# Performance work log

Hardware: AMD Instinct MI355X
Metric: run time of the kernel (lower is better)

## Reference

```python
import math
import jax, jax.numpy as jnp
import numpy as np

COLORS = 10
MAX_SHIFT = 5
B, H, W = 32, 128, 128

_shifts = [(dy, dx) for dy in range(-MAX_SHIFT, MAX_SHIFT + 1)
           for dx in range(-MAX_SHIFT, MAX_SHIFT + 1)
           if not (dy == 0 and dx == 0)]  # include_identity=False
DYS = jnp.asarray(np.array([s[0] for s in _shifts], dtype=np.int32))
DXS = jnp.asarray(np.array([s[1] for s in _shifts], dtype=np.int32))


def _shift_all(grid):
    """Apply every (dy,dx) shift to an int grid [B,H,W] with zero padding.

    out[s, b, y, x] = grid[b, y-dy_s, x-dx_s] if in-bounds else 0,
    exactly matching apply_shift_batch (uncovered regions are color 0).
    Returns [S, B, H, W].
    """
    b, h, w = grid.shape
    padded = jnp.pad(grid, ((0, 0), (MAX_SHIFT, MAX_SHIFT), (MAX_SHIFT, MAX_SHIFT)))
    def one(dy, dx):
        return jax.lax.dynamic_slice(padded, (0, MAX_SHIFT - dy, MAX_SHIFT - dx), (b, h, w))
    return jax.vmap(one)(DYS, DXS)


def setup_inputs() -> dict:
    key = jax.random.key(0)
    k1, k2, k3 = jax.random.split(key, 3)
    return {
        "demo_in": jax.random.randint(k1, (B, H, W), 0, COLORS, dtype=jnp.int32),
        "demo_out": jax.random.randint(k2, (B, H, W), 0, COLORS, dtype=jnp.int32),
        "query_in": jax.random.randint(k3, (B, H, W), 0, COLORS, dtype=jnp.int32),
        "color_log_weight": jnp.zeros((COLORS,), dtype=jnp.float32),
        "logit_scale": jnp.asarray(4.0, dtype=jnp.float32),
    }


def reference(demo_in, demo_out, query_in, color_log_weight, logit_scale):
    b, h, w = query_in.shape
    S = DYS.shape[0]

    # Per-shift correlation score. one_hot(shifted)*one_hot(demo_out)*w summed
    # over (C,H,W) == sum over pixels of w[demo_out] * (shifted == demo_out).
    shifted_demo = _shift_all(demo_in)                       # [S,B,H,W] int
    w_out = jnp.exp(color_log_weight)[demo_out]              # [B,H,W]
    eq = (shifted_demo == demo_out[None]).astype(jnp.float32)
    match = jnp.sum(eq * w_out[None], axis=(2, 3))           # [S,B]
    scale = jnp.minimum(jnp.exp(logit_scale), 100.0)
    scores = match.T / math.sqrt(h * w) * scale              # [B,S]
    attention = jax.nn.softmax(scores, axis=1)               # [B,S]

    # Weighted accumulation of one-hot shifted queries, done as a scatter-add
    # into the color channel (avoids materializing [S,B,C,H,W]).
    shifted_query = _shift_all(query_in)                     # [S,B,H,W] int
    b_idx = jnp.arange(b)[None, :, None, None]
    y_idx = jnp.arange(h)[None, None, :, None]
    x_idx = jnp.arange(w)[None, None, None, :]
    attn_b = jnp.broadcast_to(attention.T[:, :, None, None], (S, b, h, w))
    accum = jnp.zeros((b, COLORS, h, w), dtype=jnp.float32)
    accum = accum.at[b_idx, shifted_query, y_idx, x_idx].add(attn_b)
    return jnp.log(jnp.maximum(accum, 1e-6))
```

## Files before the change

### kernel.cpp

```cpp
#include <hip/hip_runtime.h>
#include <hip/hip_bf16.h>
#include <math.h>

#define COLORS 10
#define NB 32
#define H 128
#define W 128
#define NS 120
#define HW (H*W)
#define STRIPS 8
#define SH 16
#define DROWS 26
#define DINW 12

typedef unsigned char u8;
typedef unsigned int u32;
typedef unsigned long long u64;
typedef float f32x4 __attribute__((ext_vector_type(4)));
typedef short bf16x8 __attribute__((ext_vector_type(8)));

__global__ __launch_bounds__(512) void match_strip(
    const int* __restrict__ demo_in, const int* __restrict__ demo_out,
    const float* __restrict__ clw, float* __restrict__ mpart)
{
    __shared__ __align__(16) u32 din_p[COLORS][DROWS][DINW];
    __shared__ __align__(16) u32 dout_p[COLORS][SH][4];
    __shared__ float wexp[COLORS];

    int t = threadIdx.x;
    int strip = blockIdx.x;
    int b = blockIdx.y;
    int wave = t >> 6, lane = t & 63;

    if (t < COLORS) wexp[t] = __expf(clw[t]);

    const int* di = demo_in  + b * HW;
    const int* dd = demo_out + b * HW;
    int y0 = strip * SH;

    for (int r = wave; r < DROWS; r += 8) {
        int gy = y0 - 5 + r;
        bool ok = (gy >= 0 && gy < H);
        int v0 = 0, v1 = 0;
        if (ok) { v0 = di[gy * W + lane]; v1 = di[gy * W + 64 + lane]; }
        #pragma unroll
        for (int c = 0; c < COLORS; c++) {
            u64 h0 = __ballot(v0 == c);
            u64 h1 = __ballot(v1 == c);
            u64 P0, P1, P2;
            if (!ok) {
                P0 = (c == 0) ? ~0ull : 0ull;
                P1 = P0;
                P2 = (c == 0) ? 0x3FFull : 0ull;
            } else {
                u64 lm = (c == 0) ? 0x1Full  : 0ull;
                u64 rm = (c == 0) ? 0x3E0ull : 0ull;
                P0 = (h0 << 5) | lm;
                P1 = (h0 >> 59) | (h1 << 5);
                P2 = (h1 >> 59) | rm;
            }
            if (lane == 0) {
                *reinterpret_cast<uint4*>(&din_p[c][r][0]) =
                    make_uint4((u32)P0, (u32)(P0 >> 32), (u32)P1, (u32)(P1 >> 32));
                *reinterpret_cast<uint4*>(&din_p[c][r][4]) =
                    make_uint4((u32)P2, 0u, 0u, 0u);
            }
        }
    }
    for (int r = wave; r < SH; r += 8) {
        int gy = y0 + r;
        int v0 = dd[gy * W + lane], v1 = dd[gy * W + 64 + lane];
        #pragma unroll
        for (int c = 0; c < COLORS; c++) {
            u64 h0 = __ballot(v0 == c);
            u64 h1 = __ballot(v1 == c);
            if (lane == 0)
                *reinterpret_cast<uint4*>(&dout_p[c][r][0]) =
                    make_uint4((u32)h0, (u32)(h0 >> 32), (u32)h1, (u32)(h1 >> 32));
        }
    }
    __syncthreads();

    int s = t >> 2, q = t & 3;
    float acc = 0.f;
    if (t < 4 * NS) {
        int lin = s + (s >= 60);
        int dy = lin / 11 - 5, dx = lin % 11 - 5;
        int k = 5 - dx;
        for (int c = 0; c < COLORS; c++) {
            int cnt = 0;
            #pragma unroll
            for (int yy = 0; yy < 4; yy++) {
                int y = q * 4 + yy;
                int r = y - dy + 5;
                const u32* dr   = &din_p[c][r][0];
                const u32* orow = &dout_p[c][y][0];
                u32 s0 = __builtin_amdgcn_alignbit(dr[1], dr[0], k);
                u32 s1 = __builtin_amdgcn_alignbit(dr[2], dr[1], k);
                u32 s2 = __builtin_amdgcn_alignbit(dr[3], dr[2], k);
                u32 s3 = __builtin_amdgcn_alignbit(dr[4], dr[3], k);
                cnt += __popc(s0 & orow[0]) + __popc(s1 & orow[1])
                     + __popc(s2 & orow[2]) + __popc(s3 & orow[3]);
            }
            acc += wexp[c] * (float)cnt;
        }
    }
    acc += __shfl_down(acc, 1, 64);
    acc += __shfl_down(acc, 2, 64);
    if (q == 0 && t < 4 * NS)
        mpart[(b * NS + s) * STRIPS + strip] = acc;
}

#define AR 18
__global__ __launch_bounds__(512) void accum_fused(
    const int* __restrict__ query_in, const float* __restrict__ mpart,
    const float* __restrict__ logit_scale, float* __restrict__ out)
{
    __shared__ u8  qs[AR][144];
    __shared__ float sm[NS];
    __shared__ unsigned short abf[128];
    __shared__ __align__(16) u32 Agl[11][64][4];

    int t  = threadIdx.x;
    int y0 = blockIdx.x * 8;
    int b  = blockIdx.y;
    const int* q = query_in + b * HW;

    u32 pk0 = 0, pk1 = 0;
    {
        int g = t;
        #pragma unroll
        for (int e = 0; e < 4; e++) {
            int idx = g * 4 + e;
            int r = idx / 144, p = idx - r * 144;
            int gy = y0 - 5 + r;
            bool ok = (gy >= 0) & (gy < H) & (p >= 5) & (p < 133);
            int cy = gy < 0 ? 0 : (gy > 127 ? 127 : gy);
            int cx = p < 5 ? 0 : (p > 132 ? 127 : p - 5);
            int v = q[cy * W + cx];
            pk0 |= (u32)(ok ? v : 0) << (8 * e);
        }
    }
    if (t < 648 - 512) {
        int g = t + 512;
        #pragma unroll
        for (int e = 0; e < 4; e++) {
            int idx = g * 4 + e;
            int r = idx / 144, p = idx - r * 144;
            int gy = y0 - 5 + r;
            bool ok = (gy >= 0) & (gy < H) & (p >= 5) & (p < 133);
            int cy = gy < 0 ? 0 : (gy > 127 ? 127 : gy);
            int cx = p < 5 ? 0 : (p > 132 ? 127 : p - 5);
            int v = q[cy * W + cx];
            pk1 |= (u32)(ok ? v : 0) << (8 * e);
        }
    }

    float scale = fminf(__expf(logit_scale[0]), 100.0f) * (1.0f / 128.0f);
    if (t < NS) {
        const float* mp = mpart + (t + b * NS) * STRIPS;
        float4 v0 = *reinterpret_cast<const float4*>(mp);
        float4 v1 = *reinterpret_cast<const float4*>(mp + 4);
        sm[t] = (v0.x + v0.y + v0.z + v0.w + v1.x + v1.y + v1.z + v1.w) * scale;
    }

    ((u32*)qs)[t] = pk0;
    if (t < 648 - 512) ((u32*)qs)[t + 512] = pk1;
    __syncthreads();

    if (t < 64) {
        float s0 = sm[t];
        float s1 = (t + 64 < NS) ? sm[t + 64] : -INFINITY;
        float m = fmaxf(s0, s1);
        for (int off = 32; off > 0; off >>= 1) m = fmaxf(m, __shfl_xor(m, off, 64));
        float e0 = __expf(s0 - m);
        float e1 = (t + 64 < NS) ? __expf(s1 - m) : 0.f;
        float sum = e0 + e1;
        for (int off = 32; off > 0; off >>= 1) sum += __shfl_xor(sum, off, 64);
        float inv = 1.0f / sum;
        sm[t] = e0 * inv;
        if (t + 64 < NS) sm[t + 64] = e1 * inv;
    }
    __syncthreads();
    if (t < 128) {
        unsigned short v = 0;
        if (t < 121 && t != 60) {
            int si = t - (t > 60);
            __hip_bfloat16 hb = __float2bfloat16(sm[si]);
            v = *reinterpret_cast<unsigned short*>(&hb);
        }
        abf[t] = v;
    }
    __syncthreads();

    {
        int e = t;
        int st = e >> 6, l = e & 63;
        int mrow = l & 15, g8 = (l >> 4) * 8;
        #pragma unroll
        for (int p = 0; p < 4; p++) {
            int j0 = mrow + 10 - (g8 + p * 2);
            int j1 = j0 - 1;
            int i0 = (j0 >= 0 && j0 <= 10) ? (10 - st) * 11 + j0 : 121;
            int i1 = (j1 >= 0 && j1 <= 10) ? (10 - st) * 11 + j1 : 121;
            Agl[st][l][p] = (u32)abf[i0] | ((u32)abf[i1] << 16);
        }
    }
    if (t < 704 - 512) {
        int e = t + 512;
        int st = e >> 6, l = e & 63;
        int mrow = l & 15, g8 = (l >> 4) * 8;
        #pragma unroll
        for (int p = 0; p < 4; p++) {
            int j0 = mrow + 10 - (g8 + p * 2);
            int j1 = j0 - 1;
            int i0 = (j0 >= 0 && j0 <= 10) ? (10 - st) * 11 + j0 : 121;
            int i1 = (j1 >= 0 && j1 <= 10) ? (10 - st) * 11 + j1 : 121;
            Agl[st][l][p] = (u32)abf[i0] | ((u32)abf[i1] << 16);
        }
    }
    __syncthreads();

    int lane = t & 63, w = t >> 6;
    int x0 = w * 16;
    int c = lane & 15, g = lane >> 4;

    #define BUILD_B(r) ({                                                        \
        u64 eight = *reinterpret_cast<const u64*>(&qs[(r)][x0 + 8 * g]);         \
        u32 lo = (u32)eight, hi = (u32)(eight >> 32);                            \
        u32 b0 = ((int)(lo & 255) == c ? 0x3F80u : 0u)                           \
               | ((int)((lo >> 8)  & 255) == c ? 0x3F800000u : 0u);              \
        u32 b1 = ((int)((lo >> 16) & 255) == c ? 0x3F80u : 0u)                   \
               | ((int)((lo >> 24) & 255) == c ? 0x3F800000u : 0u);              \
        u32 b2 = ((int)(hi & 255) == c ? 0x3F80u : 0u)                           \
               | ((int)((hi >> 8)  & 255) == c ? 0x3F800000u : 0u);              \
        u32 b3 = ((int)((hi >> 16) & 255) == c ? 0x3F80u : 0u)                   \
               | ((int)((hi >> 24) & 255) == c ? 0x3F800000u : 0u);              \
        make_uint4(b0, b1, b2, b3); })

    uint4 bf[8];
    #pragma unroll
    for (int r = 0; r < 7; r++) bf[r & 7] = BUILD_B(r);

    f32x4 acc0[4], acc1[4];
    #pragma unroll
    for (int j = 0; j < 4; j++) { acc0[j] = (f32x4){0,0,0,0}; acc1[j] = (f32x4){0,0,0,0}; }

    #pragma unroll
    for (int st = 0; st < 11; st++) {
        bf[(st + 7) & 7] = BUILD_B(st + 7);
        uint4 a4 = *reinterpret_cast<const uint4*>(&Agl[st][lane][0]);
        union { uint4 u; bf16x8 v; } A; A.u = a4;
        #pragma unroll
        for (int j = 0; j < 4; j++) {
            union { uint4 u; bf16x8 v; } B0, B1;
            B0.u = bf[(st + j) & 7];
            B1.u = bf[(st + 4 + j) & 7];
            acc0[j] = __builtin_amdgcn_mfma_f32_16x16x32_bf16(A.v, B0.v, acc0[j], 0, 0, 0);
            acc1[j] = __builtin_amdgcn_mfma_f32_16x16x32_bf16(A.v, B1.v, acc1[j], 0, 0, 0);
        }
    }
    #undef BUILD_B

    if (c < COLORS) {
        #pragma unroll
        for (int j = 0; j < 4; j++) {
            float* ob0 = out + (((size_t)b * COLORS + c) * H + (y0 + j)) * W + x0 + 4 * g;
            float4 r0;
            r0.x = __logf(fmaxf(acc0[j][0], 1e-6f));
            r0.y = __logf(fmaxf(acc0[j][1], 1e-6f));
            r0.z = __logf(fmaxf(acc0[j][2], 1e-6f));
            r0.w = __logf(fmaxf(acc0[j][3], 1e-6f));
            *reinterpret_cast<float4*>(ob0) = r0;
            float* ob1 = out + (((size_t)b * COLORS + c) * H + (y0 + 4 + j)) * W + x0 + 4 * g;
            float4 r1;
            r1.x = __logf(fmaxf(acc1[j][0], 1e-6f));
            r1.y = __logf(fmaxf(acc1[j][1], 1e-6f));
            r1.z = __logf(fmaxf(acc1[j][2], 1e-6f));
            r1.w = __logf(fmaxf(acc1[j][3], 1e-6f));
            *reinterpret_cast<float4*>(ob1) = r1;
        }
    }
}

__global__ __launch_bounds__(256) void match_kernel(
    const int* __restrict__ demo_in, const int* __restrict__ demo_out,
    const float* __restrict__ clw, float* __restrict__ match)
{
    int blk = blockIdx.x;
    int b = blk / NS;
    int s = blk % NS;
    int lin = s + (s >= 60 ? 1 : 0);
    int dy = lin / 11 - 5, dx = lin % 11 - 5;

    __shared__ float wexp[COLORS];
    int tid = threadIdx.x;
    if (tid < COLORS) wexp[tid] = expf(clw[tid]);
    __syncthreads();

    const int* __restrict__ din  = demo_in  + b * HW;
    const int* __restrict__ dout = demo_out + b * HW;

    float partial = 0.f;
    for (int i = tid; i < HW; i += 256) {
        int yy = i >> 7, xx = i & 127;
        int co = dout[i];
        int sy = yy - dy, sx = xx - dx;
        int v = 0;
        if (sy >= 0 && sy < H && sx >= 0 && sx < W) v = din[sy * W + sx];
        if (v == co) partial += wexp[co];
    }
    for (int off = 32; off > 0; off >>= 1) partial += __shfl_down(partial, off, 64);
    __shared__ float wsum[4];
    if ((tid & 63) == 0) wsum[tid >> 6] = partial;
    __syncthreads();
    if (tid == 0) match[blk] = wsum[0] + wsum[1] + wsum[2] + wsum[3];
}

__global__ __launch_bounds__(64) void softmax_kernel(
    const float* __restrict__ match, const float* __restrict__ logit_scale,
    float* __restrict__ attention)
{
    int b = blockIdx.x;
    int lane = threadIdx.x;
    float scale = fminf(expf(logit_scale[0]), 100.0f) / sqrtf((float)HW);
    int i0 = lane, i1 = lane + 64;
    float s0 = match[b * NS + i0] * scale;
    float s1 = (i1 < NS) ? match[b * NS + i1] * scale : -INFINITY;
    float m = fmaxf(s0, s1);
    for (int off = 32; off > 0; off >>= 1) m = fmaxf(m, __shfl_xor(m, off, 64));
    float e0 = expf(s0 - m);
    float e1 = (i1 < NS) ? expf(s1 - m) : 0.f;
    float sum = e0 + e1;
    for (int off = 32; off > 0; off >>= 1) sum += __shfl_xor(sum, off, 64);
    float inv = 1.0f / sum;
    attention[b * NS + i0] = e0 * inv;
    if (i1 < NS) attention[b * NS + i1] = e1 * inv;
}

__global__ __launch_bounds__(128) void accum_kernel(
    const int* __restrict__ query_in, const float* __restrict__ attention,
    float* __restrict__ out)
{
    int blk = blockIdx.x;
    int b = blk >> 7;
    int y = blk & 127;
    int x = threadIdx.x;

    __shared__ float att[NS];
    if (threadIdx.x < NS) att[threadIdx.x] = attention[b * NS + threadIdx.x];
    __syncthreads();

    const int* __restrict__ q = query_in + b * HW;
    float acc[COLORS];
    #pragma unroll
    for (int c = 0; c < COLORS; c++) acc[c] = 0.f;

    #pragma unroll 4
    for (int s = 0; s < NS; s++) {
        int lin = s + (s >= 60 ? 1 : 0);
        int dy = lin / 11 - 5, dx = lin % 11 - 5;
        int sy = y - dy, sx = x - dx;
        int v = 0;
        if (sy >= 0 && sy < H && sx >= 0 && sx < W) v = q[sy * W + sx];
        float a = att[s];
        #pragma unroll
        for (int c = 0; c < COLORS; c++) acc[c] += (v == c) ? a : 0.f;
    }
    float* __restrict__ ob = out + (size_t)b * COLORS * HW + y * W + x;
    #pragma unroll
    for (int c = 0; c < COLORS; c++) ob[c * HW] = __logf(fmaxf(acc[c], 1e-6f));
}

extern "C" void kernel_launch(void* const* d_in, const int* in_sizes, int n_in,
                              void* d_out, int out_size, void* d_ws, size_t ws_size,
                              hipStream_t stream) {
    const int*   demo_in     = (const int*)d_in[0];
    const int*   demo_out    = (const int*)d_in[1];
    const int*   query_in    = (const int*)d_in[2];
    const float* clw         = (const float*)d_in[3];
    const float* logit_scale = (const float*)d_in[4];
    float* out = (float*)d_out;

    size_t needed = (size_t)NB * NS * STRIPS * sizeof(float);

    if (ws_size >= needed) {
        float* mpart = (float*)d_ws;
        match_strip<<<dim3(STRIPS, NB), 512, 0, stream>>>(demo_in, demo_out, clw, mpart);
        accum_fused<<<dim3(H / 8, NB), 512, 0, stream>>>(query_in, mpart, logit_scale, out);
    } else {
        float* match = (float*)d_ws;
        float* att   = match + NB * NS;
        match_kernel<<<NB * NS, 256, 0, stream>>>(demo_in, demo_out, clw, match);
        softmax_kernel<<<NB, 64, 0, stream>>>(match, logit_scale, att);
        accum_kernel<<<NB * H, 128, 0, stream>>>(query_in, att, out);
    }
}
```

Baseline: 28.65 us.

## Restructure match kernel so each thread computes all dx shifts from register rows

```diff
diff --git a/kernel.cpp b/kernel.cpp
--- a/kernel.cpp
+++ b/kernel.cpp
@@ -12,6 +12,7 @@
 #define SH 16
 #define DROWS 26
 #define DINW 12
+#define AR 18
 
 typedef unsigned char u8;
 typedef unsigned int u32;
@@ -31,12 +32,12 @@
     int strip = blockIdx.x;
     int b = blockIdx.y;
     int wave = t >> 6, lane = t & 63;
+    int y0 = strip * SH;
 
     if (t < COLORS) wexp[t] = __expf(clw[t]);
 
     const int* di = demo_in  + b * HW;
     const int* dd = demo_out + b * HW;
-    int y0 = strip * SH;
 
     for (int r = wave; r < DROWS; r += 8) {
         int gy = y0 - 5 + r;
@@ -81,37 +82,60 @@
     }
     __syncthreads();
 
-    int s = t >> 2, q = t & 3;
-    float acc = 0.f;
-    if (t < 4 * NS) {
-        int lin = s + (s >= 60);
-        int dy = lin / 11 - 5, dx = lin % 11 - 5;
-        int k = 5 - dx;
-        for (int c = 0; c < COLORS; c++) {
-            int cnt = 0;
+    float acc[11];
+    #pragma unroll
+    for (int i = 0; i < 11; i++) acc[i] = 0.f;
+
+    if (t < 352) {
+        int dyIdx = t >> 5;
+        int ch    = (t >> 4) & 1;
+        int y     = t & 15;
+        int r     = y - dyIdx + 10;
+
+        #pragma unroll
+        for (int cc = 0; cc < 5; cc++) {
+            int c = ch * 5 + cc;
+            const u32* dr = &din_p[c][r][0];
+            u32 d0 = dr[0], d1 = dr[1], d2 = dr[2], d3 = dr[3], d4 = dr[4];
+            const u32* orw = &dout_p[c][y][0];
+            u32 o0 = orw[0], o1 = orw[1], o2 = orw[2], o3 = orw[3];
+            float wgt = wexp[c];
             #pragma unroll
-            for (int yy = 0; yy < 4; yy++) {
-                int y = q * 4 + yy;
-                int r = y - dy + 5;
-                const u32* dr   = &din_p[c][r][0];
-                const u32* orow = &dout_p[c][y][0];
-                u32 s0 = __builtin_amdgcn_alignbit(dr[1], dr[0], k);
-                u32 s1 = __builtin_amdgcn_alignbit(dr[2], dr[1], k);
-                u32 s2 = __builtin_amdgcn_alignbit(dr[3], dr[2], k);
-                u32 s3 = __builtin_amdgcn_alignbit(dr[4], dr[3], k);
-                cnt += __popc(s0 & orow[0]) + __popc(s1 & orow[1])
-                     + __popc(s2 & orow[2]) + __popc(s3 & orow[3]);
+            for (int dxi = 0; dxi < 11; dxi++) {
+                int k = 10 - dxi;
+                u32 s0 = __builtin_amdgcn_alignbit(d1, d0, k);
+                u32 s1 = __builtin_amdgcn_alignbit(d2, d1, k);
+                u32 s2 = __builtin_amdgcn_alignbit(d3, d2, k);
+                u32 s3 = __builtin_amdgcn_alignbit(d4, d3, k);
+                int cnt = __popc(s0 & o0) + __popc(s1 & o1)
+                        + __popc(s2 & o2) + __popc(s3 & o3);
+                acc[dxi] += wgt * (float)cnt;
             }
-            acc += wexp[c] * (float)cnt;
-        }
-    }
-    acc += __shfl_down(acc, 1, 64);
-    acc += __shfl_down(acc, 2, 64);
-    if (q == 0 && t < 4 * NS)
-        mpart[(b * NS + s) * STRIPS + strip] = acc;
-}
-
-#define AR 18
+        }
+    }
+
+    #pragma unroll
+    for (int dxi = 0; dxi < 11; dxi++) {
+        float v = acc[dxi];
+        v += __shfl_down(v, 16, 32);
+        v += __shfl_down(v, 8, 32);
+        v += __shfl_down(v, 4, 32);
+        v += __shfl_down(v, 2, 32);
+        v += __shfl_down(v, 1, 32);
+        acc[dxi] = v;
+    }
+    if ((t & 31) == 0 && t < 352) {
+        int dyIdx = t >> 5;
+        #pragma unroll
+        for (int dxi = 0; dxi < 11; dxi++) {
+            int lin = dyIdx * 11 + dxi;
+            if (lin == 60) continue;
+            int s = lin - (lin > 60);
+            mpart[(b * NS + s) * STRIPS + strip] = acc[dxi];
+        }
+    }
+}
+
 __global__ __launch_bounds__(512) void accum_fused(
     const int* __restrict__ query_in, const float* __restrict__ mpart,
     const float* __restrict__ logit_scale, float* __restrict__ out)
```

Measured after the change: 29.47 us. +2.9%, slower.
